# Kernel tuning notes

Hardware: AMD Instinct MI355X
Metric: run time of the kernel (lower is better)

Reference implementation:

```python
import jax, jax.numpy as jnp
import numpy as np

DIM = 256; HEADS = 4; HD = DIM // HEADS; SCALE = HD ** -0.5
CBS = 4; CSTRIDE = 2; SBS = 4; NSEL = 16; WS = 7
B = 4; H = 64; W = 64


def _unfold(x, bs, stride):
    # x: (B,H,W,C) -> (B, nh*nw, C*bs*bs), flat channel order matches torch F.unfold
    # (index = c*bs*bs + kh*bs + kw)
    b, h, w, c = x.shape
    nh = (h - bs) // stride + 1
    nw = (w - bs) // stride + 1
    cols = [x[:, kh:kh + nh * stride:stride, kw:kw + nw * stride:stride, :]
            for kh in range(bs) for kw in range(bs)]
    p = jnp.stack(cols, axis=-1)  # (B,nh,nw,C,bs*bs)
    return p.reshape(b, nh * nw, c * bs * bs)


def _rel_pos_index(ws):
    coords = np.stack(np.meshgrid(np.arange(ws), np.arange(ws), indexing='ij')).reshape(2, -1)
    rel = (coords[:, :, None] - coords[:, None, :]).transpose(1, 2, 0).copy()
    rel[:, :, 0] += ws - 1
    rel[:, :, 1] += ws - 1
    rel[:, :, 0] *= 2 * ws - 1
    return jnp.asarray(rel.sum(-1))  # (ws*ws, ws*ws) int


def _mlp(x, w1, b1, w2, b2):
    return jax.nn.gelu(x @ w1 + b1, approximate=False) @ w2 + b2


def _window_attn(x, qkv_w, qkv_b, proj_w, proj_b, bias_table):
    b, c, h, w = x.shape
    ws = WS
    ph = (ws - h % ws) % ws
    pw = (ws - w % ws) % ws
    xp = jnp.pad(x, ((0, 0), (0, 0), (0, ph), (0, pw)))
    hp, wp = h + ph, w + pw
    xw = xp.reshape(b, c, hp // ws, ws, wp // ws, ws).transpose(0, 2, 4, 3, 5, 1).reshape(-1, ws * ws, c)
    bw = xw.shape[0]
    qkv = (xw @ qkv_w + qkv_b).reshape(bw, ws * ws, 3, HEADS, HD).transpose(2, 0, 3, 1, 4)
    q, k, v = qkv[0], qkv[1], qkv[2]
    attn = jnp.einsum('bhnd,bhmd->bhnm', q, k) * SCALE
    rpi = _rel_pos_index(ws)
    bias = bias_table[rpi.reshape(-1)].reshape(ws * ws, ws * ws, HEADS).transpose(2, 0, 1)
    attn = jax.nn.softmax(attn + bias[None], axis=-1)
    o = jnp.einsum('bhnm,bhmd->bhnd', attn, v).transpose(0, 2, 1, 3).reshape(bw, ws * ws, c)
    o = o @ proj_w + proj_b
    o = o.reshape(b, hp // ws, wp // ws, ws, ws, c).transpose(0, 5, 1, 3, 2, 4).reshape(b, c, hp, wp)
    return o[:, :, :h, :w]


def _forward(x, qkv_cmp_w, qkv_cmp_b, qkv_slc_w, qkv_slc_b,
             cmpk_w1, cmpk_b1, cmpk_w2, cmpk_b2,
             cmpv_w1, cmpv_b1, cmpv_w2, cmpv_b2, pos_embed,
             win_qkv_w, win_qkv_b, win_proj_w, win_proj_b, win_bias_table,
             proj_cmp_w, proj_cmp_b, proj_slc_w, proj_slc_b,
             gate_w1, gate_b1, gate_w2, gate_b2):
    b, c, h, w = x.shape
    n = h * w
    xs = x.reshape(b, c, n).transpose(0, 2, 1)  # (B,N,C)

    # --- compressed branch ---
    qkv = (xs @ qkv_cmp_w + qkv_cmp_b).reshape(b, n, 3, HEADS, HD).transpose(2, 0, 3, 1, 4)
    q_c, k_c, v_c = qkv[0], qkv[1], qkv[2]  # (B,heads,N,hd)
    k_flat = k_c.transpose(0, 2, 1, 3).reshape(b, n, c)
    v_flat = v_c.transpose(0, 2, 1, 3).reshape(b, n, c)
    fk = _unfold(k_flat.reshape(b, h, w, c), CBS, CSTRIDE)  # (B,nb,C*16)
    fv = _unfold(v_flat.reshape(b, h, w, c), CBS, CSTRIDE)
    nb = fk.shape[1]
    # replicate torch's reshape of the channel-major unfold vector into (bs*bs, dim)
    kpos = (fk.reshape(b, nb, CBS * CBS, c) + pos_embed[None]).reshape(b, nb, CBS * CBS * c)
    k_cmp = _mlp(kpos, cmpk_w1, cmpk_b1, cmpk_w2, cmpk_b2)  # (B,nb,C)
    v_cmp = _mlp(fv, cmpv_w1, cmpv_b1, cmpv_w2, cmpv_b2)
    kch = k_cmp.reshape(b, nb, HEADS, HD).transpose(0, 2, 1, 3)
    vch = v_cmp.reshape(b, nb, HEADS, HD).transpose(0, 2, 1, 3)
    attn_cmp = jax.nn.softmax(jnp.einsum('bhnd,bhmd->bhnm', q_c, kch) * SCALE, axis=-1)
    out_cmp = jnp.einsum('bhnm,bhmd->bhnd', attn_cmp, vch).transpose(0, 2, 1, 3).reshape(b, n, c)
    out_cmp = out_cmp @ proj_cmp_w + proj_cmp_b

    # --- selected branch ---
    qkv2 = (xs @ qkv_slc_w + qkv_slc_b).reshape(b, n, 3, HEADS, HD).transpose(2, 0, 3, 1, 4)
    q_s, k_s, v_s = qkv2[0], qkv2[1], qkv2[2]
    ks_flat = k_s.transpose(0, 2, 1, 3).reshape(b, n, c)
    vs_flat = v_s.transpose(0, 2, 1, 3).reshape(b, n, c)
    imp = attn_cmp.sum(axis=1).mean(axis=1)  # (B, nb)
    ns = min(NSEL, nb)
    _, idx = jax.lax.top_k(imp, ns)
    fkb = _unfold(ks_flat.reshape(b, h, w, c), SBS, SBS)
    fvb = _unfold(vs_flat.reshape(b, h, w, c), SBS, SBS)
    nb2 = fkb.shape[1]
    kb = fkb.reshape(b, nb2, SBS * SBS, c)
    vb = fvb.reshape(b, nb2, SBS * SBS, c)
    idx = jnp.clip(idx, 0, nb2 - 1)
    k_slc = jnp.take_along_axis(kb, idx[:, :, None, None], axis=1).reshape(b, ns * SBS * SBS, c)
    v_slc = jnp.take_along_axis(vb, idx[:, :, None, None], axis=1).reshape(b, ns * SBS * SBS, c)
    ksh = k_slc.reshape(b, -1, HEADS, HD).transpose(0, 2, 1, 3)
    vsh = v_slc.reshape(b, -1, HEADS, HD).transpose(0, 2, 1, 3)
    attn_slc = jax.nn.softmax(jnp.einsum('bhnd,bhmd->bhnm', q_s, ksh) * SCALE, axis=-1)
    out_slc = jnp.einsum('bhnm,bhmd->bhnd', attn_slc, vsh).transpose(0, 2, 1, 3).reshape(b, n, c)
    out_slc = out_slc @ proj_slc_w + proj_slc_b

    # --- window branch ---
    out_win = _window_attn(x, win_qkv_w, win_qkv_b, win_proj_w, win_proj_b, win_bias_table)
    out_win = out_win.reshape(b, c, n).transpose(0, 2, 1)

    # --- gated combination ---
    g = jax.nn.sigmoid(jax.nn.gelu(xs @ gate_w1 + gate_b1, approximate=False) @ gate_w2 + gate_b2)
    out = g[..., 0:1] * out_cmp + g[..., 1:2] * out_slc + g[..., 2:3] * out_win
    return out.transpose(0, 2, 1).reshape(b, c, h, w)


def setup_inputs() -> dict:
    key = jax.random.key(0)
    ks = jax.random.split(key, 16)
    s = 0.02
    d = {
        'x': jax.random.normal(ks[0], (B, DIM, H, W), jnp.float32),
        'qkv_cmp_w': jax.random.normal(ks[1], (DIM, 3 * DIM)) * s,
        'qkv_cmp_b': jnp.zeros((3 * DIM,)),
        'qkv_slc_w': jax.random.normal(ks[2], (DIM, 3 * DIM)) * s,
        'qkv_slc_b': jnp.zeros((3 * DIM,)),
        'cmpk_w1': jax.random.normal(ks[3], (DIM * CBS * CBS, 2 * DIM)) * s,
        'cmpk_b1': jnp.zeros((2 * DIM,)),
        'cmpk_w2': jax.random.normal(ks[4], (2 * DIM, DIM)) * s,
        'cmpk_b2': jnp.zeros((DIM,)),
        'cmpv_w1': jax.random.normal(ks[5], (DIM * CBS * CBS, 2 * DIM)) * s,
        'cmpv_b1': jnp.zeros((2 * DIM,)),
        'cmpv_w2': jax.random.normal(ks[6], (2 * DIM, DIM)) * s,
        'cmpv_b2': jnp.zeros((DIM,)),
        'pos_embed': jax.random.normal(ks[7], (1, CBS * CBS, DIM)) * s,
        'win_qkv_w': jax.random.normal(ks[8], (DIM, 3 * DIM)) * s,
        'win_qkv_b': jnp.zeros((3 * DIM,)),
        'win_proj_w': jax.random.normal(ks[9], (DIM, DIM)) * s,
        'win_proj_b': jnp.zeros((DIM,)),
        'win_bias_table': jax.random.normal(ks[10], ((2 * WS - 1) ** 2, HEADS)) * s,
        'proj_cmp_w': jax.random.normal(ks[11], (DIM, DIM)) * s,
        'proj_cmp_b': jnp.zeros((DIM,)),
        'proj_slc_w': jax.random.normal(ks[12], (DIM, DIM)) * s,
        'proj_slc_b': jnp.zeros((DIM,)),
        'gate_w1': jax.random.normal(ks[13], (DIM, DIM // 4)) * s,
        'gate_b1': jnp.zeros((DIM // 4,)),
        'gate_w2': jax.random.normal(ks[14], (DIM // 4, 3)) * s,
        'gate_b2': jnp.zeros((3,)),
    }
    return d


def reference(x, qkv_cmp_w, qkv_cmp_b, qkv_slc_w, qkv_slc_b,
              cmpk_w1, cmpk_b1, cmpk_w2, cmpk_b2,
              cmpv_w1, cmpv_b1, cmpv_w2, cmpv_b2, pos_embed,
              win_qkv_w, win_qkv_b, win_proj_w, win_proj_b, win_bias_table,
              proj_cmp_w, proj_cmp_b, proj_slc_w, proj_slc_b,
              gate_w1, gate_b1, gate_w2, gate_b2):
    return _forward(x, qkv_cmp_w, qkv_cmp_b, qkv_slc_w, qkv_slc_b,
                    cmpk_w1, cmpk_b1, cmpk_w2, cmpk_b2,
                    cmpv_w1, cmpv_b1, cmpv_w2, cmpv_b2, pos_embed,
                    win_qkv_w, win_qkv_b, win_proj_w, win_proj_b, win_bias_table,
                    proj_cmp_w, proj_cmp_b, proj_slc_w, proj_slc_b,
                    gate_w1, gate_b1, gate_w2, gate_b2)
```

## Files before the change

kernel.cpp:

```cpp
#include <hip/hip_runtime.h>
#include <stdint.h>
#include <stddef.h>


#define DEV __device__ __forceinline__

typedef __attribute__((ext_vector_type(8))) short short8;
typedef __attribute__((ext_vector_type(4))) float f32x4;
typedef unsigned short u16;

DEV u16 f2bf(float f){
    unsigned u = __float_as_uint(f);
    u += 0x7FFFu + ((u>>16)&1u);
    return (u16)(u>>16);
}
DEV float bf2f(u16 u){ return __uint_as_float(((unsigned)u)<<16); }

#define LGKM0() asm volatile("s_waitcnt lgkmcnt(0)" ::: "memory")

__global__ void k_xs(const float* __restrict__ x, u16* __restrict__ xh,
                     u16* __restrict__ xl){
    __shared__ float t[32][33];
    int b = blockIdx.z; int c0 = blockIdx.y*32; int n0 = blockIdx.x*32;
    int tx = threadIdx.x, ty = threadIdx.y;
    for(int i=ty;i<32;i+=8)
        t[i][tx] = x[((size_t)(b*256 + c0+i))*4096 + n0 + tx];
    __syncthreads();
    for(int i=ty;i<32;i+=8){
        float v = t[tx][i];
        u16 h = f2bf(v);
        size_t o = ((size_t)(b*4096 + n0+i))*256 + c0 + tx;
        xh[o] = h;
        xl[o] = f2bf(v - bf2f(h));
    }
}

__global__ void k_wt(const float* __restrict__ W, u16* __restrict__ WT,
                     int K, int N){
    __shared__ float t[32][33];
    int k0 = blockIdx.x*32, n0 = blockIdx.y*32;
    int tx = threadIdx.x, ty = threadIdx.y;
    for(int i=ty;i<32;i+=8)
        if(k0+i<K && n0+tx<N) t[i][tx] = W[(size_t)(k0+i)*N + n0+tx];
    __syncthreads();
    for(int i=ty;i<32;i+=8)
        if(n0+i<N && k0+tx<K) WT[(size_t)(n0+i)*K + k0+tx] = f2bf(t[tx][i]);
}

__global__ void k_wt2(const float* __restrict__ W, u16* __restrict__ Hi,
                      u16* __restrict__ Lo, int K, int N){
    __shared__ float t[32][33];
    int k0 = blockIdx.x*32, n0 = blockIdx.y*32;
    int tx = threadIdx.x, ty = threadIdx.y;
    for(int i=ty;i<32;i+=8)
        if(k0+i<K && n0+tx<N) t[i][tx] = W[(size_t)(k0+i)*N + n0+tx];
    __syncthreads();
    for(int i=ty;i<32;i+=8)
        if(n0+i<N && k0+tx<K){
            float v = t[tx][i];
            u16 h = f2bf(v);
            Hi[(size_t)(n0+i)*K + k0+tx] = h;
            Lo[(size_t)(n0+i)*K + k0+tx] = f2bf(v - bf2f(h));
        }
}

__global__ void k_vt(const float* __restrict__ vc, u16* __restrict__ vt,
                     int NK, int ldk){
    __shared__ float t[32][33];
    int b = blockIdx.z; int k0 = blockIdx.x*32; int c0 = blockIdx.y*32;
    int tx = threadIdx.x, ty = threadIdx.y;
    for(int i=ty;i<32;i+=8){
        int k = k0+i;
        t[i][tx] = (k < NK) ? vc[((size_t)(b*NK + k))*256 + c0 + tx] : 0.f;
    }
    __syncthreads();
    for(int i=ty;i<32;i+=8){
        int k = k0+tx;
        if(k < ldk)
            vt[((size_t)(b*256 + c0+i))*ldk + k] = f2bf(t[tx][i]);
    }
}

__global__ __launch_bounds__(256) void k_gemm(
        const float* __restrict__ A, const float* __restrict__ W,
        const float* __restrict__ bias, float* __restrict__ C,
        int M, int K, int Nn, int act)
{
    __shared__ float As[16][68];
    __shared__ float Bs[16][64];
    const int m0 = blockIdx.y*64, n0 = blockIdx.x*64;
    const int t = threadIdx.x, tx = t&15, ty = t>>4;
    float acc[4][4] = {};
    const int am = t>>2;
    const int ak = (t&3)*4;
    const bool arow_ok = (m0+am) < M;

    for(int k0=0;k0<K;k0+=16){
        float4 av = make_float4(0.f,0.f,0.f,0.f);
        if(arow_ok) av = *reinterpret_cast<const float4*>(&A[(size_t)(m0+am)*K + k0 + ak]);
        As[ak+0][am]=av.x; As[ak+1][am]=av.y; As[ak+2][am]=av.z; As[ak+3][am]=av.w;
        {
            int n = t&63, kb = t>>6;
            #pragma unroll
            for(int r=0;r<4;r++){
                int kk = r*4 + kb; float v = 0.f;
                if(n0+n < Nn) v = W[(size_t)(k0+kk)*Nn + n0+n];
                Bs[kk][n] = v;
            }
        }
        __syncthreads();
        #pragma unroll
        for(int kk=0;kk<16;kk++){
            float a0=As[kk][ty*4+0], a1=As[kk][ty*4+1], a2=As[kk][ty*4+2], a3=As[kk][ty*4+3];
            float b0=Bs[kk][tx*4+0], b1=Bs[kk][tx*4+1], b2=Bs[kk][tx*4+2], b3=Bs[kk][tx*4+3];
            acc[0][0]=fmaf(a0,b0,acc[0][0]); acc[0][1]=fmaf(a0,b1,acc[0][1]);
            acc[0][2]=fmaf(a0,b2,acc[0][2]); acc[0][3]=fmaf(a0,b3,acc[0][3]);
            acc[1][0]=fmaf(a1,b0,acc[1][0]); acc[1][1]=fmaf(a1,b1,acc[1][1]);
            acc[1][2]=fmaf(a1,b2,acc[1][2]); acc[1][3]=fmaf(a1,b3,acc[1][3]);
            acc[2][0]=fmaf(a2,b0,acc[2][0]); acc[2][1]=fmaf(a2,b1,acc[2][1]);
            acc[2][2]=fmaf(a2,b2,acc[2][2]); acc[2][3]=fmaf(a2,b3,acc[2][3]);
            acc[3][0]=fmaf(a3,b0,acc[3][0]); acc[3][1]=fmaf(a3,b1,acc[3][1]);
            acc[3][2]=fmaf(a3,b2,acc[3][2]); acc[3][3]=fmaf(a3,b3,acc[3][3]);
        }
        __syncthreads();
    }
    #pragma unroll
    for(int i=0;i<4;i++){
        int m = m0 + ty*4 + i;
        if(m >= M) continue;
        #pragma unroll
        for(int j=0;j<4;j++){
            int n = n0 + tx*4 + j;
            if(n >= Nn) continue;
            float v = acc[i][j] + (bias ? bias[n] : 0.f);
            if(act==1)      v = 0.5f*v*(1.0f + erff(v*0.70710678118654752f));
            else if(act==2) v = 1.0f/(1.0f + expf(-v));
            C[(size_t)m*Nn + n] = v;
        }
    }
}

template<int WM, int WN, int AM, int BMD, int NSPLIT, int OBF>
__global__ __launch_bounds__(256) void k_mgs(
        const float* __restrict__ Af, const u16* __restrict__ Ah,
        const u16* __restrict__ Al,
        const float* __restrict__ Bf, const u16* __restrict__ Bh,
        const u16* __restrict__ Bl,
        const float* __restrict__ bias, float* __restrict__ C,
        u16* __restrict__ Cb, u16* __restrict__ Cb2,
        int M, int N, int K, int lda, int ldb, int ldc, int act, float scale,
        long zsA, long zsB, long zsC)
{
    constexpr int BM = 32*WM, BN = 32*WN;
    constexpr bool SP = (NSPLIT == 3);
    const long zo = (long)blockIdx.z;
    if(AM==0){ Af += zo*zsA; } else { Ah += zo*zsA; if(AM==2) Al += zo*zsA; }
    if(BMD==0){ Bf += zo*zsB; } else { Bh += zo*zsB; if(BMD==2) Bl += zo*zsB; }
    if(OBF) Cb += zo*zsC; else C += zo*zsC;

    __shared__ u16 Ahi[BM*64];
    __shared__ u16 Alo[SP ? BM*64 : 8];
    __shared__ u16 Bhi[BN*64];
    __shared__ u16 Blo[SP ? BN*64 : 8];

    const int m0 = blockIdx.y*BM, n0 = blockIdx.x*BN;
    const int tid = threadIdx.x, lane = tid&63, wv = tid>>6;
    const int wm = (wv>>1)*(16*WM), wn = (wv&1)*(16*WN);
    f32x4 acc[WM][WN] = {};

    constexpr int TPR_A = 256/BM;
    constexpr int CH_A  = 8/TPR_A;
    const int arow = tid / TPR_A;
    const int acol0 = (tid % TPR_A)*(128/TPR_A);
    constexpr int TPR_B = 256/BN;
    constexpr int CH_B  = 8/TPR_B;
    const int brow = tid / TPR_B;
    const int bcol0 = (tid % TPR_B)*(128/TPR_B);

    for(int kt=0; kt<K; kt+=64){
        {
            const bool ok = (m0+arow) < M;
            #pragma unroll
            for(int c=0;c<CH_A;c++){
                int colbyte = acol0 + c*16;
                int e = colbyte>>1;
                const bool lok = ok && (kt + e + 8 <= K);
                short8 h = {}, l = {};
                if(AM==0){
                    float4 v0 = make_float4(0,0,0,0), v1 = v0;
                    if(lok){
                        const float* src = &Af[(size_t)(m0+arow)*lda + kt + e];
                        v0 = *reinterpret_cast<const float4*>(src);
                        v1 = *reinterpret_cast<const float4*>(src+4);
                    }
                    float vv[8] = {v0.x,v0.y,v0.z,v0.w,v1.x,v1.y,v1.z,v1.w};
                    #pragma unroll
                    for(int j=0;j<8;j++){
                        u16 hb = f2bf(vv[j]);
                        h[j] = (short)hb;
                        if(SP) l[j] = (short)f2bf(vv[j] - bf2f(hb));
                    }
                } else {
                    if(lok){
                        h = *reinterpret_cast<const short8*>(Ah + (size_t)(m0+arow)*lda + kt + e);
                        if(SP && AM==2)
                            l = *reinterpret_cast<const short8*>(Al + (size_t)(m0+arow)*lda + kt + e);
                    }
                }
                int byteoff = arow*128 + (colbyte ^ ((arow&7)<<4));
                *reinterpret_cast<short8*>(reinterpret_cast<char*>(Ahi)+byteoff) = h;
                if(SP)
                    *reinterpret_cast<short8*>(reinterpret_cast<char*>(Alo)+byteoff) = l;
            }
        }
        {
            const bool ok = (n0+brow) < N;
            #pragma unroll
            for(int c=0;c<CH_B;c++){
                int colbyte = bcol0 + c*16;
                int e = colbyte>>1;
                const bool lok = ok && (kt + e + 8 <= K);
                short8 h = {}, l = {};
                if(BMD==0){
                    float4 v0 = make_float4(0,0,0,0), v1 = v0;
                    if(lok){
                        const float* src = &Bf[(size_t)(n0+brow)*ldb + kt + e];
                        v0 = *reinterpret_cast<const float4*>(src);
                        v1 = *reinterpret_cast<const float4*>(src+4);
                    }
                    float vv[8] = {v0.x,v0.y,v0.z,v0.w,v1.x,v1.y,v1.z,v1.w};
                    #pragma unroll
                    for(int j=0;j<8;j++){
                        u16 hb = f2bf(vv[j]);
                        h[j] = (short)hb;
                        if(SP) l[j] = (short)f2bf(vv[j] - bf2f(hb));
                    }
                } else {
                    if(lok){
                        h = *reinterpret_cast<const short8*>(Bh + (size_t)(n0+brow)*ldb + kt + e);
                        if(SP && BMD==2)
                            l = *reinterpret_cast<const short8*>(Bl + (size_t)(n0+brow)*ldb + kt + e);
                    }
                }
                int byteoff = brow*128 + (colbyte ^ ((brow&7)<<4));
                *reinterpret_cast<short8*>(reinterpret_cast<char*>(Bhi)+byteoff) = h;
                if(SP)
                    *reinterpret_cast<short8*>(reinterpret_cast<char*>(Blo)+byteoff) = l;
            }
        }
        __syncthreads();
        __builtin_amdgcn_s_setprio(1);
        #pragma unroll
        for(int kb=0;kb<2;kb++){
            short8 ah[WM], al[WM], bh[WN], bl[WN];
            #pragma unroll
            for(int i=0;i<WM;i++){
                int ar = wm + i*16 + (lane&15);
                int ab = ar*128 + (((kb*64) + ((lane>>4)*16)) ^ ((ar&7)<<4));
                ah[i] = *reinterpret_cast<const short8*>(reinterpret_cast<const char*>(Ahi)+ab);
                if(SP)
                    al[i] = *reinterpret_cast<const short8*>(reinterpret_cast<const char*>(Alo)+ab);
            }
            #pragma unroll
            for(int i=0;i<WN;i++){
                int br = wn + i*16 + (lane&15);
                int bb = br*128 + (((kb*64) + ((lane>>4)*16)) ^ ((br&7)<<4));
                bh[i] = *reinterpret_cast<const short8*>(reinterpret_cast<const char*>(Bhi)+bb);
                if(SP)
                    bl[i] = *reinterpret_cast<const short8*>(reinterpret_cast<const char*>(Blo)+bb);
            }
            #pragma unroll
            for(int mi=0;mi<WM;mi++)
                #pragma unroll
                for(int ni=0;ni<WN;ni++){
                    if(SP){
                        acc[mi][ni] = __builtin_amdgcn_mfma_f32_16x16x32_bf16(
                                          al[mi], bh[ni], acc[mi][ni], 0, 0, 0);
                        acc[mi][ni] = __builtin_amdgcn_mfma_f32_16x16x32_bf16(
                                          ah[mi], bl[ni], acc[mi][ni], 0, 0, 0);
                    }
                    acc[mi][ni] = __builtin_amdgcn_mfma_f32_16x16x32_bf16(
                                      ah[mi], bh[ni], acc[mi][ni], 0, 0, 0);
                }
        }
        __builtin_amdgcn_s_setprio(0);
        __syncthreads();
    }
    #pragma unroll
    for(int mi=0;mi<WM;mi++){
        #pragma unroll
        for(int ni=0;ni<WN;ni++){
            int col = n0 + wn + ni*16 + (lane&15);
            if(col >= N) continue;
            int rowb = m0 + wm + mi*16 + ((lane>>4)*4);
            float bv = bias ? bias[col] : 0.f;
            #pragma unroll
            for(int r=0;r<4;r++){
                int m = rowb + r;
                if(m >= M) continue;
                float v = acc[mi][ni][r]*scale + bv;
                if(act==1)      v = 0.5f*v*(1.0f + erff(v*0.70710678118654752f));
                else if(act==2) v = 1.0f/(1.0f + expf(-v));
                if(OBF==2){
                    u16 hb = f2bf(v);
                    Cb [(size_t)m*ldc + col] = hb;
                    Cb2[(size_t)m*ldc + col] = f2bf(v - bf2f(hb));
                } else if(OBF==1){
                    Cb[(size_t)m*ldc + col] = f2bf(v);
                } else {
                    C [(size_t)m*ldc + col] = v;
                }
            }
        }
    }
}

template<int SPLIT, int IMP, int NKR, int NT, int LDV>
__global__ __launch_bounds__(256) void k_fattn(
    const float* __restrict__ Qg, const u16* __restrict__ Khg,
    const u16* __restrict__ Klg, const u16* __restrict__ VTg,
    float* __restrict__ Og, float* __restrict__ impp)
{
    const int qb = blockIdx.x, h = blockIdx.y, b = blockIdx.z;
    const int tid = threadIdx.x, lane = tid&63, wv = tid>>6;
    const int wm = wv*16;
    const int rgrp = lane>>4;
    const int cidx = lane&15;

    __shared__ u16 Qh[64*64];
    __shared__ u16 Ql[SPLIT?64*64:8];
    __shared__ u16 Kh[64*64];
    __shared__ u16 Kl[SPLIT?64*64:8];
    __shared__ u16 Pl[64*64];
    __shared__ u16 Vl[64*64];
    __shared__ float part[4][64];
    __shared__ float colacc[IMP? NT*64 : 8];

    const int srow = tid>>2;
    const int scol0 = (tid&3)*32;

    short8 kh_r[2], kl_r[2], v_r[2];

    auto LK = [&](int t){
        const bool ok = (t*64 + srow) < NKR;
        const u16* srch = &Khg[((size_t)b*NKR + t*64 + srow)*256 + h*64];
        const u16* srcl = SPLIT ? &Klg[((size_t)b*NKR + t*64 + srow)*256 + h*64] : nullptr;
        #pragma unroll
        for(int c=0;c<2;c++){
            int e = (scol0 + c*16)>>1;
            short8 hh = {}, ll = {};
            if(ok){
                hh = *reinterpret_cast<const short8*>(srch+e);
                if(SPLIT) ll = *reinterpret_cast<const short8*>(srcl+e);
            }
            kh_r[c] = hh;
            if(SPLIT) kl_r[c] = ll;
        }
    };
    auto WK = [&](){
        #pragma unroll
        for(int c=0;c<2;c++){
            int colbyte = scol0 + c*16;
            int byteoff = srow*128 + (colbyte ^ ((srow&7)<<4));
            *reinterpret_cast<short8*>(reinterpret_cast<char*>(Kh)+byteoff) = kh_r[c];
            if(SPLIT)
                *reinterpret_cast<short8*>(reinterpret_cast<char*>(Kl)+byteoff) = kl_r[c];
        }
    };
    auto LV = [&](int t){
        const u16* src = &VTg[((size_t)b*256 + h*64 + srow)*LDV + t*64];
        #pragma unroll
        for(int c=0;c<2;c++){
            int e = (scol0 + c*16)>>1;
            short8 hh = {};
            if(t*64 + e + 8 <= LDV)
                hh = *reinterpret_cast<const short8*>(src + e);
            v_r[c] = hh;
        }
    };
    auto WV = [&](){
        #pragma unroll
        for(int c=0;c<2;c++){
            int colbyte = scol0 + c*16;
            int byteoff = srow*128 + (colbyte ^ ((srow&7)<<4));
            *reinterpret_cast<short8*>(reinterpret_cast<char*>(Vl)+byteoff) = v_r[c];
        }
    };

    {
        const float* src = &Qg[((size_t)b*4096 + qb*64 + srow)*768 + h*64];
        #pragma unroll
        for(int c=0;c<2;c++){
            int colbyte = scol0 + c*16;
            int e = colbyte>>1;
            float4 v0 = *reinterpret_cast<const float4*>(src+e);
            float4 v1 = *reinterpret_cast<const float4*>(src+e+4);
            float vv[8]={v0.x,v0.y,v0.z,v0.w,v1.x,v1.y,v1.z,v1.w};
            short8 hh, ll;
            #pragma unroll
            for(int j=0;j<8;j++){
                u16 hb=f2bf(vv[j]); hh[j]=(short)hb;
                if(SPLIT) ll[j]=(short)f2bf(vv[j]-bf2f(hb));
            }
            int byteoff = srow*128 + (colbyte ^ ((srow&7)<<4));
            *reinterpret_cast<short8*>(reinterpret_cast<char*>(Qh)+byteoff)=hh;
            if(SPLIT)
                *reinterpret_cast<short8*>(reinterpret_cast<char*>(Ql)+byteoff)=ll;
        }
        if(IMP) for(int k=tid;k<NT*64;k+=256) colacc[k]=0.f;
    }

    float lsum[4] = {0.f,0.f,0.f,0.f};

    LK(0);
    for(int t=0;t<NT;t++){
        const int kt = t*64;
        LGKM0();
        __builtin_amdgcn_s_barrier();
        WK();
        if(t+1<NT) LK(t+1);
        LGKM0();
        __builtin_amdgcn_s_barrier();
        f32x4 acc[4] = {};
        __builtin_amdgcn_s_setprio(1);
        #pragma unroll
        for(int kb=0;kb<2;kb++){
            int koff = kb*64 + rgrp*16;
            int ar = wm + cidx;
            int ab = ar*128 + (koff ^ ((ar&7)<<4));
            short8 ah = *reinterpret_cast<const short8*>(reinterpret_cast<const char*>(Qh)+ab);
            short8 al;
            if(SPLIT) al = *reinterpret_cast<const short8*>(reinterpret_cast<const char*>(Ql)+ab);
            #pragma unroll
            for(int ni=0;ni<4;ni++){
                int br = ni*16 + cidx;
                int bb = br*128 + (koff ^ ((br&7)<<4));
                short8 bh = *reinterpret_cast<const short8*>(reinterpret_cast<const char*>(Kh)+bb);
                if(SPLIT){
                    short8 bl = *reinterpret_cast<const short8*>(reinterpret_cast<const char*>(Kl)+bb);
                    acc[ni] = __builtin_amdgcn_mfma_f32_16x16x32_bf16(al, bh, acc[ni], 0,0,0);
                    acc[ni] = __builtin_amdgcn_mfma_f32_16x16x32_bf16(ah, bl, acc[ni], 0,0,0);
                }
                acc[ni] = __builtin_amdgcn_mfma_f32_16x16x32_bf16(ah, bh, acc[ni], 0,0,0);
            }
        }
        __builtin_amdgcn_s_setprio(0);
        #pragma unroll
        for(int ni=0;ni<4;ni++){
            int col = kt + ni*16 + cidx;
            if(col < NKR){
                #pragma unroll
                for(int r=0;r<4;r++)
                    lsum[r] += __expf(acc[ni][r]*0.125f);
            }
        }
    }
    float inv[4];
    #pragma unroll
    for(int r=0;r<4;r++){
        float l = lsum[r];
        l += __shfl_xor(l,1); l += __shfl_xor(l,2);
        l += __shfl_xor(l,4); l += __shfl_xor(l,8);
        inv[r] = 1.f/l;
    }

    f32x4 acc_o[4] = {};
    LK(0); LV(0);
    for(int t=0;t<NT;t++){
        const int kt = t*64;
        LGKM0();
        __builtin_amdgcn_s_barrier();
        WK(); WV();
        if(t+1<NT){ LK(t+1); LV(t+1); }
        LGKM0();
        __builtin_amdgcn_s_barrier();
        f32x4 acc[4] = {};
        __builtin_amdgcn_s_setprio(1);
        #pragma unroll
        for(int kb=0;kb<2;kb++){
            int koff = kb*64 + rgrp*16;
            int ar = wm + cidx;
            int ab = ar*128 + (koff ^ ((ar&7)<<4));
            short8 ah = *reinterpret_cast<const short8*>(reinterpret_cast<const char*>(Qh)+ab);
            short8 al;
            if(SPLIT) al = *reinterpret_cast<const short8*>(reinterpret_cast<const char*>(Ql)+ab);
            #pragma unroll
            for(int ni=0;ni<4;ni++){
                int br = ni*16 + cidx;
                int bb = br*128 + (koff ^ ((br&7)<<4));
                short8 bh = *reinterpret_cast<const short8*>(reinterpret_cast<const char*>(Kh)+bb);
                if(SPLIT){
                    short8 bl = *reinterpret_cast<const short8*>(reinterpret_cast<const char*>(Kl)+bb);
                    acc[ni] = __builtin_amdgcn_mfma_f32_16x16x32_bf16(al, bh, acc[ni], 0,0,0);
                    acc[ni] = __builtin_amdgcn_mfma_f32_16x16x32_bf16(ah, bl, acc[ni], 0,0,0);
                }
                acc[ni] = __builtin_amdgcn_mfma_f32_16x16x32_bf16(ah, bh, acc[ni], 0,0,0);
            }
        }
        __builtin_amdgcn_s_setprio(0);
        float cs[4] = {0.f,0.f,0.f,0.f};
        #pragma unroll
        for(int ni=0;ni<4;ni++){
            #pragma unroll
            for(int r=0;r<4;r++){
                int col = kt + ni*16 + cidx;
                float p = 0.f;
                if(col < NKR)
                    p = __expf(acc[ni][r]*0.125f) * inv[r];
                int prow = wm + rgrp*4 + r;
                int pcol = ni*16 + cidx;
                int byteoff = prow*128 + ((pcol*2) ^ ((prow&7)<<4));
                *reinterpret_cast<u16*>(reinterpret_cast<char*>(Pl)+byteoff) = f2bf(p);
                if(IMP) cs[ni] += p;
            }
        }
        if(IMP){
            #pragma unroll
            for(int ni=0;ni<4;ni++){
                cs[ni] += __shfl_xor(cs[ni],16);
                cs[ni] += __shfl_xor(cs[ni],32);
            }
            if(rgrp==0){
                #pragma unroll
                for(int ni=0;ni<4;ni++)
                    part[wv][ni*16+cidx] = cs[ni];
            }
        }
        LGKM0();
        __builtin_amdgcn_s_barrier();
        if(IMP && tid < 64)
            colacc[kt+tid] += ((part[0][tid]+part[1][tid])+part[2][tid])+part[3][tid];
        __builtin_amdgcn_s_setprio(1);
        #pragma unroll
        for(int kb=0;kb<2;kb++){
            int koff = kb*64 + rgrp*16;
            int ar = wm + cidx;
            int ab = ar*128 + (koff ^ ((ar&7)<<4));
            short8 pa = *reinterpret_cast<const short8*>(reinterpret_cast<const char*>(Pl)+ab);
            #pragma unroll
            for(int ni=0;ni<4;ni++){
                int br = ni*16 + cidx;
                int bb = br*128 + (koff ^ ((br&7)<<4));
                short8 vb = *reinterpret_cast<const short8*>(reinterpret_cast<const char*>(Vl)+bb);
                acc_o[ni] = __builtin_amdgcn_mfma_f32_16x16x32_bf16(pa, vb, acc_o[ni], 0,0,0);
            }
        }
        __builtin_amdgcn_s_setprio(0);
    }
    __syncthreads();
    #pragma unroll
    for(int ni=0;ni<4;ni++){
        #pragma unroll
        for(int r=0;r<4;r++){
            int q = qb*64 + wm + rgrp*4 + r;
            int d = ni*16 + cidx;
            Og[((size_t)b*4096 + q)*256 + h*64 + d] = acc_o[ni][r];
        }
    }
    if(IMP){
        size_t base = ((size_t)((b*4+h)*64) + qb)*976;
        for(int k=tid; k<NT*64 && k<976; k+=256)
            impp[base+k] = colacc[k];
    }
}

__global__ void k_unfold2(const float* __restrict__ qkv, const float* __restrict__ pos,
                          u16* __restrict__ kh, u16* __restrict__ kl,
                          u16* __restrict__ vv){
    int row = blockIdx.x;
    int b = row / 961, blk = row % 961;
    int bi = blk / 31, bj = blk % 31;
    for(int j = threadIdx.x; j < 4096; j += 256){
        int ch = j >> 4;
        int khh = (j >> 2) & 3, kw = j & 3;
        int n = (bi*2 + khh)*64 + (bj*2 + kw);
        size_t base = ((size_t)(b*4096) + n)*768 + ch;
        float kv = qkv[base + 256] + pos[j];
        float va = qkv[base + 512];
        u16 h = f2bf(kv);
        kh[(size_t)row*4096 + j] = h;
        kl[(size_t)row*4096 + j] = f2bf(kv - bf2f(h));
        vv[(size_t)row*4096 + j] = f2bf(va);
    }
}

__global__ void k_imp_reduce(const float* __restrict__ impp, float* __restrict__ imp){
    __shared__ float part[4][64];
    int b = blockIdx.y;
    int k = blockIdx.x*64 + (threadIdx.x & 63);
    int rr = threadIdx.x >> 6;
    float s = 0.f;
    if(k < 976){
        for(int r=rr; r<256; r+=4)
            s += impp[((size_t)(b*256) + r)*976 + k];
    }
    part[rr][threadIdx.x & 63] = s;
    __syncthreads();
    if(threadIdx.x < 64 && k < 961){
        float t = ((part[0][threadIdx.x] + part[1][threadIdx.x])
                 + part[2][threadIdx.x]) + part[3][threadIdx.x];
        imp[b*961 + k] = t;
    }
}

__global__ __launch_bounds__(256) void k_topk(const float* __restrict__ imp,
                                              int* __restrict__ idx){
    int b = blockIdx.x;
    __shared__ float v[961];
    __shared__ float wvv[4];
    __shared__ int   wvi[4];
    int t = threadIdx.x;
    int lane = t & 63, wid = t >> 6;
    for(int i=t;i<961;i+=256) v[i] = imp[b*961+i];
    __syncthreads();
    for(int it=0; it<16; it++){
        float bv = -1e30f; int bi = 1<<30;
        for(int i=t;i<961;i+=256){
            float val = v[i];
            if(val > bv){ bv=val; bi=i; }
        }
        #pragma unroll
        for(int off=32; off>0; off>>=1){
            float ov = __shfl_xor(bv, off);
            int   oi = __shfl_xor(bi, off);
            if(ov > bv || (ov == bv && oi < bi)){ bv = ov; bi = oi; }
        }
        if(lane==0){ wvv[wid]=bv; wvi[wid]=bi; }
        __syncthreads();
        if(t==0){
            float gb=wvv[0]; int gi=wvi[0];
            #pragma unroll
            for(int w=1;w<4;w++){
                if(wvv[w]>gb || (wvv[w]==gb && wvi[w]<gi)){ gb=wvv[w]; gi=wvi[w]; }
            }
            idx[b*16+it] = gi;
            v[gi] = -1e30f;
        }
        __syncthreads();
    }
}

__global__ void k_gather_sel(const float* __restrict__ qkv2, const int* __restrict__ idx,
                             u16* __restrict__ Ks, float* __restrict__ Vs){
    int row = blockIdx.x;
    int b = row >> 8, tt = row & 255;
    int sel = tt >> 4, p = tt & 15;
    int blk = idx[b*16+sel]; if(blk > 255) blk = 255;
    int bi = blk >> 4, bj = blk & 15;
    int cc = threadIdx.x;
    int y = bi*4 + ((cc>>2)&3), xx = bj*4 + (cc&3);
    int ch = p*16 + (cc>>4);
    size_t src = ((size_t)(b*4096) + y*64 + xx)*768;
    Ks[(size_t)row*256 + cc] = f2bf(qkv2[src + 256 + ch]);
    Vs[(size_t)row*256 + cc] = qkv2[src + 512 + ch];
}

__global__ void k_xw(const u16* __restrict__ xh, u16* __restrict__ xw){
    int row = blockIdx.x;
    int wb = row / 49, t = row % 49;
    int b = wb / 100, wrem = wb % 100;
    int wy = wrem / 10, wx = wrem % 10;
    int ty = t / 7, tx = t % 7;
    int y = wy*7 + ty, xx = wx*7 + tx;
    int c = threadIdx.x;
    u16 v = 0;
    if(y < 64 && xx < 64) v = xh[((size_t)(b*4096) + y*64 + xx)*256 + c];
    xw[(size_t)row*256 + c] = v;
}

__global__ __launch_bounds__(64) void k_attn_win(
    const u16* __restrict__ qkvw, const float* __restrict__ btab,
    u16* __restrict__ outp)
{
    const int wb = blockIdx.x, h = blockIdx.y;
    const int lane = threadIdx.x;
    __shared__ float lk[49][64];
    __shared__ float lv[49][64];
    __shared__ float ls[49][51];
    __shared__ float lbias[169];
    for(int i=lane;i<169;i+=64) lbias[i] = btab[i*4 + h];
    for(int r=0;r<49;r++){
        lk[r][lane] = bf2f(qkvw[((size_t)(wb*49 + r))*768 + 256 + h*64 + lane]);
        lv[r][lane] = bf2f(qkvw[((size_t)(wb*49 + r))*768 + 512 + h*64 + lane]);
    }
    __syncthreads();
    if(lane < 49){
        const u16* qptr = &qkvw[((size_t)(wb*49 + lane))*768 + h*64];
        float qreg[64];
        #pragma unroll
        for(int d=0;d<64;++d) qreg[d] = bf2f(qptr[d]);
        int ih = lane/7, iw = lane%7;
        float m = -1e30f;
        for(int j=0;j<49;j++){
            float s0=0,s1=0,s2=0,s3=0;
            #pragma unroll
            for(int d=0; d<64; d+=4){
                s0 = fmaf(qreg[d+0], lk[j][d+0], s0);
                s1 = fmaf(qreg[d+1], lk[j][d+1], s1);
                s2 = fmaf(qreg[d+2], lk[j][d+2], s2);
                s3 = fmaf(qreg[d+3], lk[j][d+3], s3);
            }
            int jh=j/7, jw=j%7;
            float s = ((s0+s1)+(s2+s3))*0.125f + lbias[(ih-jh+6)*13 + (iw-jw+6)];
            ls[lane][j] = s;
            m = fmaxf(m, s);
        }
        float l = 0.f;
        for(int j=0;j<49;j++){ float p = __expf(ls[lane][j] - m); ls[lane][j] = p; l += p; }
        float inv = 1.f/l;
        u16* op = &outp[((size_t)(wb*49 + lane))*256 + h*64];
        for(int d=0;d<64;d++){
            float a0=0,a1=0;
            for(int j=0;j<48;j+=2){
                a0 = fmaf(ls[lane][j],   lv[j][d],   a0);
                a1 = fmaf(ls[lane][j+1], lv[j+1][d], a1);
            }
            a0 = fmaf(ls[lane][48], lv[48][d], a0);
            op[d] = f2bf((a0+a1)*inv);
        }
    }
}

__global__ void k_combine(const float* __restrict__ ocp, const float* __restrict__ osp,
                          const float* __restrict__ owp, const float* __restrict__ g,
                          float* __restrict__ out){
    __shared__ float tile[32][33];
    int b = blockIdx.z; int c0 = blockIdx.y*32, n0 = blockIdx.x*32;
    int tx = threadIdx.x, ty = threadIdx.y;
    for(int i=ty;i<32;i+=8){
        int n = n0 + i;
        float g0 = g[(size_t)(b*4096+n)*3 + 0];
        float g1 = g[(size_t)(b*4096+n)*3 + 1];
        float g2 = g[(size_t)(b*4096+n)*3 + 2];
        int y = n >> 6, xx = n & 63;
        int wy = y/7, ty2 = y%7, wx = xx/7, tx2 = xx%7;
        size_t wrow = (size_t)(b*100 + wy*10 + wx)*49 + ty2*7 + tx2;
        size_t base = ((size_t)(b*4096) + n)*256 + c0;
        float vc = ocp[base + tx];
        float vs = osp[base + tx];
        float vw = owp[wrow*256 + c0 + tx];
        tile[i][tx] = g0*vc + g1*vs + g2*vw;
    }
    __syncthreads();
    for(int i=ty;i<32;i+=8)
        out[((size_t)(b*256 + c0+i))*4096 + n0 + tx] = tile[tx][i];
}

extern "C" void kernel_launch(void* const* d_in, const int* in_sizes, int n_in,
                              void* d_out, int out_size, void* d_ws, size_t ws_size,
                              hipStream_t stream)
{
    typedef const float* fp;
    fp x          = (fp)d_in[0];
    fp qkv_cmp_w  = (fp)d_in[1];  fp qkv_cmp_b = (fp)d_in[2];
    fp qkv_slc_w  = (fp)d_in[3];  fp qkv_slc_b = (fp)d_in[4];
    fp cmpk_w1    = (fp)d_in[5];  fp cmpk_b1   = (fp)d_in[6];
    fp cmpk_w2    = (fp)d_in[7];  fp cmpk_b2   = (fp)d_in[8];
    fp cmpv_w1    = (fp)d_in[9];  fp cmpv_b1   = (fp)d_in[10];
    fp cmpv_w2    = (fp)d_in[11]; fp cmpv_b2   = (fp)d_in[12];
    fp pos_embed  = (fp)d_in[13];
    fp win_qkv_w  = (fp)d_in[14]; fp win_qkv_b = (fp)d_in[15];
    fp win_proj_w = (fp)d_in[16]; fp win_proj_b= (fp)d_in[17];
    fp win_btab   = (fp)d_in[18];
    fp proj_cmp_w = (fp)d_in[19]; fp proj_cmp_b= (fp)d_in[20];
    fp proj_slc_w = (fp)d_in[21]; fp proj_slc_b= (fp)d_in[22];
    fp gate_w1    = (fp)d_in[23]; fp gate_b1   = (fp)d_in[24];
    fp gate_w2    = (fp)d_in[25]; fp gate_b2   = (fp)d_in[26];
    (void)in_sizes; (void)n_in; (void)out_size;

    char* ws = (char*)d_ws;
    size_t off = 0;
    auto alloc = [&](size_t bytes)->size_t{
        size_t r = off; off += (bytes + 255) & ~(size_t)255; return r;
    };
    const size_t XSH  = alloc((size_t)16384*256*2);
    const size_t XSL  = alloc((size_t)16384*256*2);
    const size_t QKV  = alloc((size_t)16384*768*4);
    const size_t BIGA = alloc((size_t)4*4096*976*4);
    const size_t HID  = alloc((size_t)3844*512*4);
    const size_t KCH  = alloc((size_t)3844*256*2);
    const size_t KCL  = alloc((size_t)3844*256*2);
    const size_t VC   = alloc((size_t)3844*256*4);
    const size_t S_IMPP = (size_t)4096*976*4;
    const size_t S_OC   = (size_t)16384*256*4;
    const size_t S_PB   = (size_t)4*4096*976*2;
    const size_t POOL = alloc(S_IMPP + S_OC + S_OC + S_PB);
    const size_t IMP  = alloc((size_t)4*961*4);
    const size_t IDX  = alloc((size_t)4*16*4);
    const size_t KS   = alloc((size_t)4*256*256*2);
    const size_t VS   = alloc((size_t)4*256*256*4);
    const size_t G2   = alloc((size_t)16384*3*4);
    const size_t VTC  = alloc((size_t)4*256*976*2);
    const size_t VTS  = alloc((size_t)4*256*256*2);
    const size_t TQS  = alloc((size_t)768*256*2);
    const size_t TWQ  = alloc((size_t)768*256*2);
    const size_t TV1  = alloc((size_t)512*4096*2);
    const size_t TV2  = alloc((size_t)256*512*2);
    const size_t TPC  = alloc((size_t)256*256*2);
    const size_t TPS  = alloc((size_t)256*256*2);
    const size_t TWP  = alloc((size_t)256*256*2);
    const size_t TG1  = alloc((size_t)64*256*2);
    const size_t TQCH = alloc((size_t)768*256*2);
    const size_t TQCL = alloc((size_t)768*256*2);
    const size_t TK1H = alloc((size_t)512*4096*2);
    const size_t TK1L = alloc((size_t)512*4096*2);
    const size_t TK2H = alloc((size_t)256*512*2);
    const size_t TK2L = alloc((size_t)256*512*2);
    if(off > ws_size) return;

    u16*   p_xsh = (u16*)(ws + XSH);
    u16*   p_xsl = (u16*)(ws + XSL);
    float* p_qkv = (float*)(ws + QKV);
    u16*   p_bigb= (u16*)  (ws + BIGA);
    u16*   p_uv  = (u16*)  (ws + BIGA);
    float* p_oslc= (float*)(ws + BIGA);
    float* p_owp = (float*)(ws + BIGA + 20971520);
    float* p_hid = (float*)(ws + HID);
    u16*   p_kch = (u16*)(ws + KCH);
    u16*   p_kcl = (u16*)(ws + KCL);
    float* p_vc  = (float*)(ws + VC);
    float* p_impp= (float*)(ws + POOL);
    float* p_oc  = (float*)(ws + POOL + S_IMPP);
    float* p_ocp = (float*)(ws + POOL + S_IMPP + S_OC);
    u16*   p_ukh = (u16*)  (ws + POOL);
    u16*   p_ukl = p_ukh + (size_t)3844*4096;
    u16*   p_xwb = (u16*)  (ws + POOL);
    u16*   p_owin= (u16*)  (ws + POOL + S_IMPP);
    float* p_imp = (float*)(ws + IMP);
    int*   p_idx = (int*)  (ws + IDX);
    u16*   p_ks  = (u16*)(ws + KS);
    float* p_vs  = (float*)(ws + VS);
    float* p_g   = (float*)(ws + G2);
    u16*   p_vtc = (u16*)(ws + VTC);
    u16*   p_vts = (u16*)(ws + VTS);
    u16* t_qs = (u16*)(ws + TQS);
    u16* t_wq = (u16*)(ws + TWQ);
    u16* t_v1 = (u16*)(ws + TV1);
    u16* t_v2 = (u16*)(ws + TV2);
    u16* t_pc = (u16*)(ws + TPC);
    u16* t_ps = (u16*)(ws + TPS);
    u16* t_wp = (u16*)(ws + TWP);
    u16* t_g1 = (u16*)(ws + TG1);
    u16* t_qch= (u16*)(ws + TQCH);
    u16* t_qcl= (u16*)(ws + TQCL);
    u16* t_k1h= (u16*)(ws + TK1H);
    u16* t_k1l= (u16*)(ws + TK1L);
    u16* t_k2h= (u16*)(ws + TK2H);
    u16* t_k2l= (u16*)(ws + TK2L);

    auto wt = [&](fp W, u16* WT, int K, int Nn){
        k_wt<<<dim3((K+31)/32, (Nn+31)/32), dim3(32,8), 0, stream>>>(W, WT, K, Nn);
    };
    auto wt2 = [&](fp W, u16* H, u16* L, int K, int Nn){
        k_wt2<<<dim3((K+31)/32, (Nn+31)/32), dim3(32,8), 0, stream>>>(W, H, L, K, Nn);
    };

    wt(qkv_slc_w, t_qs, 256, 768);
    wt(win_qkv_w, t_wq, 256, 768);
    wt(cmpv_w1,   t_v1, 4096, 512);
    wt(cmpv_w2,   t_v2, 512, 256);
    wt(proj_cmp_w,t_pc, 256, 256);
    wt(proj_slc_w,t_ps, 256, 256);
    wt(win_proj_w,t_wp, 256, 256);
    wt(gate_w1,   t_g1, 256, 64);
    wt2(qkv_cmp_w, t_qch, t_qcl, 256, 768);
    wt2(cmpk_w1,   t_k1h, t_k1l, 4096, 512);
    wt2(cmpk_w2,   t_k2h, t_k2l, 512, 256);

    k_xs<<<dim3(128,8,4), dim3(32,8), 0, stream>>>(x, p_xsh, p_xsl);
    k_mgs<4,4,2,2,3,0><<<dim3(6,128), 256, 0, stream>>>(
        nullptr, p_xsh, p_xsl, nullptr, t_qch, t_qcl, qkv_cmp_b, p_qkv, nullptr, nullptr,
        16384, 768, 256, 256, 256, 768, 0, 1.0f, 0, 0, 0);
    k_unfold2<<<3844, 256, 0, stream>>>(p_qkv, pos_embed, p_ukh, p_ukl, p_uv);
    k_mgs<2,2,2,2,3,0><<<dim3(8,61), 256, 0, stream>>>(
        nullptr, p_ukh, p_ukl, nullptr, t_k1h, t_k1l, cmpk_b1, p_hid, nullptr, nullptr,
        3844, 512, 4096, 4096, 4096, 512, 1, 1.0f, 0, 0, 0);
    k_mgs<2,2,0,2,3,2><<<dim3(4,61), 256, 0, stream>>>(
        p_hid, nullptr, nullptr, nullptr, t_k2h, t_k2l, cmpk_b2, nullptr, p_kch, p_kcl,
        3844, 256, 512, 512, 512, 256, 0, 1.0f, 0, 0, 0);
    k_mgs<2,2,1,1,1,0><<<dim3(8,61), 256, 0, stream>>>(
        nullptr, p_uv, nullptr, nullptr, t_v1, nullptr, cmpv_b1, p_hid, nullptr, nullptr,
        3844, 512, 4096, 4096, 4096, 512, 1, 1.0f, 0, 0, 0);
    k_mgs<2,2,0,1,1,0><<<dim3(4,61), 256, 0, stream>>>(
        p_hid, nullptr, nullptr, nullptr, t_v2, nullptr, cmpv_b2, p_vc, nullptr, nullptr,
        3844, 256, 512, 512, 512, 256, 0, 1.0f, 0, 0, 0);
    k_vt<<<dim3(31,8,4), dim3(32,8), 0, stream>>>(p_vc, p_vtc, 961, 976);
    k_fattn<1,1,961,16,976><<<dim3(64,4,4), 256, 0, stream>>>(
        p_qkv, p_kch, p_kcl, p_vtc, p_oc, p_impp);
    k_imp_reduce<<<dim3(16,4), 256, 0, stream>>>(p_impp, p_imp);
    k_topk<<<4, 256, 0, stream>>>(p_imp, p_idx);
    k_mgs<4,4,0,1,1,0><<<dim3(2,128), 256, 0, stream>>>(
        p_oc, nullptr, nullptr, nullptr, t_pc, nullptr, proj_cmp_b, p_ocp, nullptr, nullptr,
        16384, 256, 256, 256, 256, 256, 0, 1.0f, 0, 0, 0);
    k_mgs<4,4,1,1,1,0><<<dim3(6,128), 256, 0, stream>>>(
        nullptr, p_xsh, nullptr, nullptr, t_qs, nullptr, qkv_slc_b, p_qkv, nullptr, nullptr,
        16384, 768, 256, 256, 256, 768, 0, 1.0f, 0, 0, 0);
    k_xw<<<19600, 256, 0, stream>>>(p_xsh, p_xwb);
    k_mgs<4,4,1,1,1,1><<<dim3(6,154), 256, 0, stream>>>(
        nullptr, p_xwb, nullptr, nullptr, t_wq, nullptr, win_qkv_b, nullptr, p_bigb, nullptr,
        19600, 768, 256, 256, 256, 768, 0, 1.0f, 0, 0, 0);
    k_attn_win<<<dim3(400,4), 64, 0, stream>>>(p_bigb, win_btab, p_owin);
    k_mgs<4,4,1,1,1,0><<<dim3(2,154), 256, 0, stream>>>(
        nullptr, p_owin, nullptr, nullptr, t_wp, nullptr, win_proj_b, p_owp, nullptr, nullptr,
        19600, 256, 256, 256, 256, 256, 0, 1.0f, 0, 0, 0);
    k_gather_sel<<<1024, 256, 0, stream>>>(p_qkv, p_idx, p_ks, p_vs);
    k_vt<<<dim3(8,8,4), dim3(32,8), 0, stream>>>(p_vs, p_vts, 256, 256);
    k_fattn<0,0,256,4,256><<<dim3(64,4,4), 256, 0, stream>>>(
        p_qkv, p_ks, nullptr, p_vts, p_oc, nullptr);
    k_mgs<4,4,0,1,1,0><<<dim3(2,128), 256, 0, stream>>>(
        p_oc, nullptr, nullptr, nullptr, t_ps, nullptr, proj_slc_b, p_oslc, nullptr, nullptr,
        16384, 256, 256, 256, 256, 256, 0, 1.0f, 0, 0, 0);
    k_mgs<2,2,1,1,1,0><<<dim3(1,256), 256, 0, stream>>>(
        nullptr, p_xsh, nullptr, nullptr, t_g1, nullptr, gate_b1, p_hid, nullptr, nullptr,
        16384, 64, 256, 256, 256, 64, 1, 1.0f, 0, 0, 0);
    k_gemm<<<dim3(1,256), 256, 0, stream>>>(p_hid, gate_w2, gate_b2, p_g,
                                            16384, 64, 3, 2);
    k_combine<<<dim3(128,8,4), dim3(32,8), 0, stream>>>(p_ocp, p_oslc, p_owp, p_g,
                                                        (float*)d_out);
}
```

Before: 816.8 us.

## Single-pass softmax for selection attention and emit bf16 attention outputs

Adds a ONEPASS mode to the fused attention kernel. In that mode the row sum is gathered during the PV pass and the output is normalised at the end, so the separate QK^T pass that only computed softmax denominators goes away; it is enabled for the selected-token attention. Without max subtraction the unnormalised exponentials rely on the scores staying small. Both attention kernels now write bf16 output, and the projection GEMMs read it as pre-converted bf16 input, which halves that traffic and skips the float-to-bf16 conversion in the GEMM at some cost in precision.

```diff
diff --git a/kernel.cpp b/kernel.cpp
--- a/kernel.cpp
+++ b/kernel.cpp
@@ -315,11 +315,11 @@
     }
 }
 
-template<int SPLIT, int IMP, int NKR, int NT, int LDV>
+template<int SPLIT, int IMP, int ONEPASS, int NKR, int NT, int LDV>
 __global__ __launch_bounds__(256) void k_fattn(
     const float* __restrict__ Qg, const u16* __restrict__ Khg,
     const u16* __restrict__ Klg, const u16* __restrict__ VTg,
-    float* __restrict__ Og, float* __restrict__ impp)
+    u16* __restrict__ Og, float* __restrict__ impp)
 {
     const int qb = blockIdx.x, h = blockIdx.y, b = blockIdx.z;
     const int tid = threadIdx.x, lane = tid&63, wv = tid>>6;
@@ -411,60 +411,62 @@
     }
 
     float lsum[4] = {0.f,0.f,0.f,0.f};
-
-    LK(0);
-    for(int t=0;t<NT;t++){
-        const int kt = t*64;
-        LGKM0();
-        __builtin_amdgcn_s_barrier();
-        WK();
-        if(t+1<NT) LK(t+1);
-        LGKM0();
-        __builtin_amdgcn_s_barrier();
-        f32x4 acc[4] = {};
-        __builtin_amdgcn_s_setprio(1);
-        #pragma unroll
-        for(int kb=0;kb<2;kb++){
-            int koff = kb*64 + rgrp*16;
-            int ar = wm + cidx;
-            int ab = ar*128 + (koff ^ ((ar&7)<<4));
-            short8 ah = *reinterpret_cast<const short8*>(reinterpret_cast<const char*>(Qh)+ab);
-            short8 al;
-            if(SPLIT) al = *reinterpret_cast<const short8*>(reinterpret_cast<const char*>(Ql)+ab);
+    float inv[4];
+    f32x4 acc_o[4] = {};
+
+    if(!ONEPASS){
+        LK(0);
+        for(int t=0;t<NT;t++){
+            const int kt = t*64;
+            LGKM0();
+            __builtin_amdgcn_s_barrier();
+            WK();
+            if(t+1<NT) LK(t+1);
+            LGKM0();
+            __builtin_amdgcn_s_barrier();
+            f32x4 acc[4] = {};
+            __builtin_amdgcn_s_setprio(1);
+            #pragma unroll
+            for(int kb=0;kb<2;kb++){
+                int koff = kb*64 + rgrp*16;
+                int ar = wm + cidx;
+                int ab = ar*128 + (koff ^ ((ar&7)<<4));
+                short8 ah = *reinterpret_cast<const short8*>(reinterpret_cast<const char*>(Qh)+ab);
+                short8 al;
+                if(SPLIT) al = *reinterpret_cast<const short8*>(reinterpret_cast<const char*>(Ql)+ab);
+                #pragma unroll
+                for(int ni=0;ni<4;ni++){
+                    int br = ni*16 + cidx;
+                    int bb = br*128 + (koff ^ ((br&7)<<4));
+                    short8 bh = *reinterpret_cast<const short8*>(reinterpret_cast<const char*>(Kh)+bb);
+                    if(SPLIT){
+                        short8 bl = *reinterpret_cast<const short8*>(reinterpret_cast<const char*>(Kl)+bb);
+                        acc[ni] = __builtin_amdgcn_mfma_f32_16x16x32_bf16(al, bh, acc[ni], 0,0,0);
+                        acc[ni] = __builtin_amdgcn_mfma_f32_16x16x32_bf16(ah, bl, acc[ni], 0,0,0);
+                    }
+                    acc[ni] = __builtin_amdgcn_mfma_f32_16x16x32_bf16(ah, bh, acc[ni], 0,0,0);
+                }
+            }
+            __builtin_amdgcn_s_setprio(0);
             #pragma unroll
             for(int ni=0;ni<4;ni++){
-                int br = ni*16 + cidx;
-                int bb = br*128 + (koff ^ ((br&7)<<4));
-                short8 bh = *reinterpret_cast<const short8*>(reinterpret_cast<const char*>(Kh)+bb);
-                if(SPLIT){
-                    short8 bl = *reinterpret_cast<const short8*>(reinterpret_cast<const char*>(Kl)+bb);
-                    acc[ni] = __builtin_amdgcn_mfma_f32_16x16x32_bf16(al, bh, acc[ni], 0,0,0);
-                    acc[ni] = __builtin_amdgcn_mfma_f32_16x16x32_bf16(ah, bl, acc[ni], 0,0,0);
+                int col = kt + ni*16 + cidx;
+                if(col < NKR){
+                    #pragma unroll
+                    for(int r=0;r<4;r++)
+                        lsum[r] += __expf(acc[ni][r]*0.125f);
                 }
-                acc[ni] = __builtin_amdgcn_mfma_f32_16x16x32_bf16(ah, bh, acc[ni], 0,0,0);
-            }
-        }
-        __builtin_amdgcn_s_setprio(0);
-        #pragma unroll
-        for(int ni=0;ni<4;ni++){
-            int col = kt + ni*16 + cidx;
-            if(col < NKR){
-                #pragma unroll
-                for(int r=0;r<4;r++)
-                    lsum[r] += __expf(acc[ni][r]*0.125f);
-            }
-        }
-    }
-    float inv[4];
-    #pragma unroll
-    for(int r=0;r<4;r++){
-        float l = lsum[r];
-        l += __shfl_xor(l,1); l += __shfl_xor(l,2);
-        l += __shfl_xor(l,4); l += __shfl_xor(l,8);
-        inv[r] = 1.f/l;
-    }
-
-    f32x4 acc_o[4] = {};
+            }
+        }
+        #pragma unroll
+        for(int r=0;r<4;r++){
+            float l = lsum[r];
+            l += __shfl_xor(l,1); l += __shfl_xor(l,2);
+            l += __shfl_xor(l,4); l += __shfl_xor(l,8);
+            inv[r] = 1.f/l;
+        }
+    }
+
     LK(0); LV(0);
     for(int t=0;t<NT;t++){
         const int kt = t*64;
@@ -505,8 +507,11 @@
             for(int r=0;r<4;r++){
                 int col = kt + ni*16 + cidx;
                 float p = 0.f;
-                if(col < NKR)
-                    p = __expf(acc[ni][r]*0.125f) * inv[r];
+                if(col < NKR){
+                    p = __expf(acc[ni][r]*0.125f);
+                    if(!ONEPASS) p *= inv[r];
+                    else lsum[r] += p;
+                }
                 int prow = wm + rgrp*4 + r;
                 int pcol = ni*16 + cidx;
                 int byteoff = prow*128 + ((pcol*2) ^ ((prow&7)<<4));
@@ -547,6 +552,15 @@
         }
         __builtin_amdgcn_s_setprio(0);
     }
+    if(ONEPASS){
+        #pragma unroll
+        for(int r=0;r<4;r++){
+            float l = lsum[r];
+            l += __shfl_xor(l,1); l += __shfl_xor(l,2);
+            l += __shfl_xor(l,4); l += __shfl_xor(l,8);
+            inv[r] = 1.f/l;
+        }
+    }
     __syncthreads();
     #pragma unroll
     for(int ni=0;ni<4;ni++){
@@ -554,7 +568,9 @@
         for(int r=0;r<4;r++){
             int q = qb*64 + wm + rgrp*4 + r;
             int d = ni*16 + cidx;
-            Og[((size_t)b*4096 + q)*256 + h*64 + d] = acc_o[ni][r];
+            float o = acc_o[ni][r];
+            if(ONEPASS) o *= inv[r];
+            Og[((size_t)b*4096 + q)*256 + h*64 + d] = f2bf(o);
         }
     }
     if(IMP){
@@ -820,7 +836,7 @@
     u16*   p_kcl = (u16*)(ws + KCL);
     float* p_vc  = (float*)(ws + VC);
     float* p_impp= (float*)(ws + POOL);
-    float* p_oc  = (float*)(ws + POOL + S_IMPP);
+    u16*   p_oc16= (u16*)  (ws + POOL + S_IMPP);
     float* p_ocp = (float*)(ws + POOL + S_IMPP + S_OC);
     u16*   p_ukh = (u16*)  (ws + POOL);
     u16*   p_ukl = p_ukh + (size_t)3844*4096;
@@ -885,12 +901,12 @@
         p_hid, nullptr, nullptr, nullptr, t_v2, nullptr, cmpv_b2, p_vc, nullptr, nullptr,
         3844, 256, 512, 512, 512, 256, 0, 1.0f, 0, 0, 0);
     k_vt<<<dim3(31,8,4), dim3(32,8), 0, stream>>>(p_vc, p_vtc, 961, 976);
-    k_fattn<1,1,961,16,976><<<dim3(64,4,4), 256, 0, stream>>>(
-        p_qkv, p_kch, p_kcl, p_vtc, p_oc, p_impp);
+    k_fattn<1,1,0,961,16,976><<<dim3(64,4,4), 256, 0, stream>>>(
+        p_qkv, p_kch, p_kcl, p_vtc, p_oc16, p_impp);
     k_imp_reduce<<<dim3(16,4), 256, 0, stream>>>(p_impp, p_imp);
     k_topk<<<4, 256, 0, stream>>>(p_imp, p_idx);
-    k_mgs<4,4,0,1,1,0><<<dim3(2,128), 256, 0, stream>>>(
-        p_oc, nullptr, nullptr, nullptr, t_pc, nullptr, proj_cmp_b, p_ocp, nullptr, nullptr,
+    k_mgs<4,4,1,1,1,0><<<dim3(2,128), 256, 0, stream>>>(
+        nullptr, p_oc16, nullptr, nullptr, t_pc, nullptr, proj_cmp_b, p_ocp, nullptr, nullptr,
         16384, 256, 256, 256, 256, 256, 0, 1.0f, 0, 0, 0);
     k_mgs<4,4,1,1,1,0><<<dim3(6,128), 256, 0, stream>>>(
         nullptr, p_xsh, nullptr, nullptr, t_qs, nullptr, qkv_slc_b, p_qkv, nullptr, nullptr,
@@ -905,10 +921,10 @@
         19600, 256, 256, 256, 256, 256, 0, 1.0f, 0, 0, 0);
     k_gather_sel<<<1024, 256, 0, stream>>>(p_qkv, p_idx, p_ks, p_vs);
     k_vt<<<dim3(8,8,4), dim3(32,8), 0, stream>>>(p_vs, p_vts, 256, 256);
-    k_fattn<0,0,256,4,256><<<dim3(64,4,4), 256, 0, stream>>>(
-        p_qkv, p_ks, nullptr, p_vts, p_oc, nullptr);
-    k_mgs<4,4,0,1,1,0><<<dim3(2,128), 256, 0, stream>>>(
-        p_oc, nullptr, nullptr, nullptr, t_ps, nullptr, proj_slc_b, p_oslc, nullptr, nullptr,
+    k_fattn<0,0,1,256,4,256><<<dim3(64,4,4), 256, 0, stream>>>(
+        p_qkv, p_ks, nullptr, p_vts, p_oc16, nullptr);
+    k_mgs<4,4,1,1,1,0><<<dim3(2,128), 256, 0, stream>>>(
+        nullptr, p_oc16, nullptr, nullptr, t_ps, nullptr, proj_slc_b, p_oslc, nullptr, nullptr,
         16384, 256, 256, 256, 256, 256, 0, 1.0f, 0, 0, 0);
     k_mgs<2,2,1,1,1,0><<<dim3(1,256), 256, 0, stream>>>(
         nullptr, p_xsh, nullptr, nullptr, t_g1, nullptr, gate_b1, p_hid, nullptr, nullptr,
```

Result: faster. 794.0 us (-2.8%).
